# Optimization experiments

Hardware: AMD Instinct MI355X
Metric: run time of the kernel (lower is better)

## Reference

```python
import jax, jax.numpy as jnp
import numpy as np

EMB_DIM = 256
N_EMBED = 1024
BETA = 0.25


def setup_inputs() -> dict:
    key = jax.random.key(0)
    k1, k2 = jax.random.split(key)
    encoderout = jax.random.normal(k1, (32, EMB_DIM, 32, 32), dtype=jnp.float32)
    # embedding.weight.data.normal_(mean=0, std=1/n_embed)
    codebook = jax.random.normal(k2, (N_EMBED, EMB_DIM), dtype=jnp.float32) * (1.0 / N_EMBED)
    return {"encoderout": encoderout, "codebook": codebook}


def reference(encoderout, codebook):
    # NCHW -> NHWC
    x = jnp.transpose(encoderout, (0, 2, 3, 1))  # [B,H,W,D]
    flat = x.reshape(-1, EMB_DIM)                # [N,D]
    d2 = (jnp.sum(flat * flat, axis=1, keepdims=True)
          + jnp.sum(codebook * codebook, axis=1)[None, :]
          - 2.0 * flat @ codebook.T)             # [N,K]
    idx = jnp.argmin(d2, axis=1)                 # [N]
    quant = codebook[idx].reshape(x.shape)       # [B,H,W,D]
    codebook_loss = jnp.mean((quant - jax.lax.stop_gradient(x)) ** 2)
    commitment_loss = jnp.mean((x - jax.lax.stop_gradient(quant)) ** 2)
    loss = codebook_loss + BETA * commitment_loss
    # FAITHFUL to source bug: straight-through output is overwritten by the
    # input permuted back to NCHW, so out == encoderout.
    out = jnp.transpose(x, (0, 3, 1, 2))
    return (out, loss, codebook_loss, commitment_loss)
```

## Files before the change

kernel.cpp:

```cpp
#include <hip/hip_runtime.h>
#include <stdint.h>

typedef short s8v __attribute__((ext_vector_type(8)));
typedef float f4v __attribute__((ext_vector_type(4)));

#define EMB_DIM 256
#define HW      1024
#define NROWS   32768
#define NELEM   (NROWS * EMB_DIM)

#define PK_OFF   0u
#define CBN_OFF  524288u
#define PSQ_OFF  528384u
#define PSM_OFF  530432u
#define DONE_OFF 532480u

__device__ __forceinline__ unsigned f2bf(float f) {
    union { float f; unsigned u; } c; c.f = f;
    unsigned u = c.u;
    return (u + 0x7FFFu + ((u >> 16) & 1u)) >> 16;
}

__global__ __launch_bounds__(256) void prep_cb(const float* __restrict__ cb,
                                               unsigned short* __restrict__ pk,
                                               float* __restrict__ cbn,
                                               unsigned* __restrict__ done) {
    int T = blockIdx.x, t = threadIdx.x;
    if (T == 0 && t == 0) *done = 0u;
    {
        int code = t >> 4, seg = t & 15;
        const float* src = cb + (size_t)(T * 16 + code) * EMB_DIM + seg * 16;
        float s2 = 0.f;
        #pragma unroll
        for (int k = 0; k < 4; ++k) {
            float4 v = *(const float4*)(src + 4 * k);
            s2 += v.x * v.x + v.y * v.y + v.z * v.z + v.w * v.w;
        }
        #pragma unroll
        for (int m = 1; m < 16; m <<= 1) s2 += __shfl_xor(s2, m, 64);
        if (seg == 0) cbn[T * 16 + code] = s2;
    }
    #pragma unroll
    for (int it = 0; it < 2; ++it) {
        int idx = t + 256 * it;
        int s = idx >> 6, l = idx & 63, G = l >> 4, ci = l & 15;
        const float* q = cb + (size_t)(T * 16 + ci) * EMB_DIM + 32 * s + 8 * G;
        float4 v0 = *(const float4*)(q);
        float4 v1 = *(const float4*)(q + 4);
        unsigned o0 = f2bf(v0.x) | (f2bf(v0.y) << 16);
        unsigned o1 = f2bf(v0.z) | (f2bf(v0.w) << 16);
        unsigned o2 = f2bf(v1.x) | (f2bf(v1.y) << 16);
        unsigned o3 = f2bf(v1.z) | (f2bf(v1.w) << 16);
        *(uint4*)((char*)pk + (size_t)T * 8192 + (size_t)idx * 16) =
            make_uint4(o0, o1, o2, o3);
    }
}

__global__ __launch_bounds__(256, 2) void vq_fused(const float* __restrict__ x,
                                                   float* __restrict__ out,
                                                   const unsigned short* __restrict__ pk,
                                                   const float* __restrict__ cbn,
                                                   float* __restrict__ psq,
                                                   float* __restrict__ psm,
                                                   unsigned* __restrict__ done) {
    __shared__ float smemf[64 * 69];
    __shared__ uint4 frag[4 * 8 * 64];
    __shared__ float mloc[4][64];
    __shared__ float red[4];
    __shared__ bool  lastf;
    __shared__ double dred[4];

    int t = threadIdx.x;
    int blk = blockIdx.x;
    int b = blk >> 4, p0 = (blk & 15) << 6;
    const float* xb = x   + (size_t)b * (EMB_DIM * HW) + p0;
    float*       ob = out + (size_t)b * (EMB_DIM * HW) + p0;

    int l = t & 63, w = t >> 6;
    int G = l >> 4, ci = l & 15;

    float sq = 0.f;
    int pq = t & 15, dd = t >> 4;
    for (int kd = 0; kd < 4; ++kd) {
        #pragma unroll
        for (int c2 = 0; c2 < 4; ++c2) {
            int dl = dd + 16 * c2;
            size_t off = (size_t)(kd * 64 + dl) * HW + 4 * pq;
            f4v v = __builtin_nontemporal_load((const f4v*)(xb + off));
            __builtin_nontemporal_store(v, (f4v*)(ob + off));
            sq += v.x * v.x + v.y * v.y + v.z * v.z + v.w * v.w;
            float* dst = &smemf[dl * 69 + 4 * pq];
            dst[0] = v.x; dst[1] = v.y; dst[2] = v.z; dst[3] = v.w;
        }
        __syncthreads();
        #pragma unroll
        for (int it = 0; it < 2; ++it) {
            int f = t + 256 * it;
            int fl = f & 63, sL = (f >> 6) & 1, R = f >> 7;
            int fG = fl >> 4, fci = fl & 15;
            const float* q = &smemf[(32 * sL + 8 * fG) * 69 + 16 * R + fci];
            unsigned o0 = f2bf(q[0])   | (f2bf(q[69])  << 16);
            unsigned o1 = f2bf(q[138]) | (f2bf(q[207]) << 16);
            unsigned o2 = f2bf(q[276]) | (f2bf(q[345]) << 16);
            unsigned o3 = f2bf(q[414]) | (f2bf(q[483]) << 16);
            frag[(R * 8 + 2 * kd + sL) * 64 + fl] = make_uint4(o0, o1, o2, o3);
        }
        __syncthreads();
    }
    #pragma unroll
    for (int m = 1; m < 64; m <<= 1) sq += __shfl_xor(sq, m, 64);
    if (l == 0) red[w] = sq;

    s8v a[4][8];
    #pragma unroll
    for (int R = 0; R < 4; ++R)
        #pragma unroll
        for (int s = 0; s < 8; ++s)
            a[R][s] = *(const s8v*)&frag[(R * 8 + s) * 64 + l];

    float mv[4][4];
    #pragma unroll
    for (int R = 0; R < 4; ++R)
        #pragma unroll
        for (int r = 0; r < 4; ++r) mv[R][r] = 1e30f;

    const char* lbase = (const char*)pk + (size_t)l * 16;
    int qbase = w * 16;
    int off = blk & 15;
    s8v cur[8], nxt[8];
    {
        const char* pt = lbase + (size_t)(qbase + off) * 8192;
        #pragma unroll
        for (int s = 0; s < 8; ++s) cur[s] = *(const s8v*)(pt + (size_t)s * 1024);
    }
    #pragma unroll 2
    for (int i = 0; i < 16; ++i) {
        int Tn = qbase + ((off + ((i + 1) & 15)) & 15);
        const char* pn = lbase + (size_t)Tn * 8192;
        #pragma unroll
        for (int s = 0; s < 8; ++s) nxt[s] = *(const s8v*)(pn + (size_t)s * 1024);

        f4v ac0 = {0.f,0.f,0.f,0.f}, ac1 = {0.f,0.f,0.f,0.f};
        f4v ac2 = {0.f,0.f,0.f,0.f}, ac3 = {0.f,0.f,0.f,0.f};
        #pragma unroll
        for (int s = 0; s < 8; ++s) {
            ac0 = __builtin_amdgcn_mfma_f32_16x16x32_bf16(a[0][s], cur[s], ac0, 0, 0, 0);
            ac1 = __builtin_amdgcn_mfma_f32_16x16x32_bf16(a[1][s], cur[s], ac1, 0, 0, 0);
            ac2 = __builtin_amdgcn_mfma_f32_16x16x32_bf16(a[2][s], cur[s], ac2, 0, 0, 0);
            ac3 = __builtin_amdgcn_mfma_f32_16x16x32_bf16(a[3][s], cur[s], ac3, 0, 0, 0);
        }
        int Tc = qbase + ((off + i) & 15);
        float cv = cbn[Tc * 16 + ci];
        #pragma unroll
        for (int r = 0; r < 4; ++r) {
            mv[0][r] = fminf(mv[0][r], cv - 2.f * ac0[r]);
            mv[1][r] = fminf(mv[1][r], cv - 2.f * ac1[r]);
            mv[2][r] = fminf(mv[2][r], cv - 2.f * ac2[r]);
            mv[3][r] = fminf(mv[3][r], cv - 2.f * ac3[r]);
        }
        #pragma unroll
        for (int s = 0; s < 8; ++s) cur[s] = nxt[s];
    }

    #pragma unroll
    for (int R = 0; R < 4; ++R)
        #pragma unroll
        for (int r = 0; r < 4; ++r) {
            float v = mv[R][r];
            #pragma unroll
            for (int m = 1; m < 16; m <<= 1) v = fminf(v, __shfl_xor(v, m, 64));
            mv[R][r] = v;
        }
    if (ci == 0) {
        #pragma unroll
        for (int R = 0; R < 4; ++R)
            #pragma unroll
            for (int r = 0; r < 4; ++r)
                mloc[w][16 * R + 4 * G + r] = mv[R][r];
    }
    __syncthreads();

    if (t < 64) {
        float m = fminf(fminf(mloc[0][t], mloc[1][t]),
                        fminf(mloc[2][t], mloc[3][t]));
        #pragma unroll
        for (int mm = 1; mm < 64; mm <<= 1) m += __shfl_xor(m, mm, 64);
        if (t == 0) {
            __hip_atomic_store(&psm[blk], m, __ATOMIC_RELAXED, __HIP_MEMORY_SCOPE_AGENT);
            __hip_atomic_store(&psq[blk], red[0] + red[1] + red[2] + red[3],
                               __ATOMIC_RELAXED, __HIP_MEMORY_SCOPE_AGENT);
            __threadfence();
            unsigned old = __hip_atomic_fetch_add(done, 1u, __ATOMIC_RELAXED,
                                                  __HIP_MEMORY_SCOPE_AGENT);
            lastf = (old == 511u);
        }
    }
    __syncthreads();

    if (lastf) {
        __threadfence();
        double s = 0.0;
        #pragma unroll
        for (int h = 0; h < 2; ++h) {
            int idx = t + 256 * h;
            s += (double)__hip_atomic_load(&psm[idx], __ATOMIC_RELAXED, __HIP_MEMORY_SCOPE_AGENT)
               + (double)__hip_atomic_load(&psq[idx], __ATOMIC_RELAXED, __HIP_MEMORY_SCOPE_AGENT);
        }
        #pragma unroll
        for (int m = 1; m < 64; m <<= 1) s += __shfl_xor(s, m, 64);
        if (l == 0) dred[w] = s;
        __syncthreads();
        if (t == 0) {
            double tot = dred[0] + dred[1] + dred[2] + dred[3];
            double cl = tot / (double)NELEM;
            out[NELEM + 0] = (float)(1.25 * cl);
            out[NELEM + 1] = (float)cl;
            out[NELEM + 2] = (float)cl;
        }
    }
}

extern "C" void kernel_launch(void* const* d_in, const int* in_sizes, int n_in,
                              void* d_out, int out_size, void* d_ws, size_t ws_size,
                              hipStream_t stream) {
    const float* enc = (const float*)d_in[0];
    const float* cb  = (const float*)d_in[1];
    float* out = (float*)d_out;

    unsigned short* pk = (unsigned short*)((char*)d_ws + PK_OFF);
    float* cbn  = (float*)((char*)d_ws + CBN_OFF);
    float* psq  = (float*)((char*)d_ws + PSQ_OFF);
    float* psm  = (float*)((char*)d_ws + PSM_OFF);
    unsigned* done = (unsigned*)((char*)d_ws + DONE_OFF);

    prep_cb<<<64, 256, 0, stream>>>(cb, pk, cbn, done);
    vq_fused<<<512, 256, 0, stream>>>(enc, out, pk, cbn, psq, psm, done);
}
```

Baseline: 115.8 us.

## Split fused VQ kernel into copy/pack and distance-argmin kernels

Splits the fused kernel into two. copy_pack loads all of its x data up front, copies it to the output, computes squared norms, and writes bf16 MFMA fragments to a workspace buffer using double-buffered shared memory. vq_dist2 reads those fragments from global memory, preloads the codebook norms into registers, and loads B fragments inline instead of software-prefetching them. The aim is to keep the memory-bound copy phase separate from the MFMA phase so each kernel has less shared memory and register pressure. The cost is an extra launch and an extra round trip through global memory for the packed activations (about 16 MB).

```diff
diff --git a/kernel.cpp b/kernel.cpp
--- a/kernel.cpp
+++ b/kernel.cpp
@@ -14,6 +14,7 @@
 #define PSQ_OFF  528384u
 #define PSM_OFF  530432u
 #define DONE_OFF 532480u
+#define XPK_OFF  1048576u
 
 __device__ __forceinline__ unsigned f2bf(float f) {
     union { float f; unsigned u; } c; c.f = f;
@@ -56,40 +57,39 @@
     }
 }
 
-__global__ __launch_bounds__(256, 2) void vq_fused(const float* __restrict__ x,
-                                                   float* __restrict__ out,
-                                                   const unsigned short* __restrict__ pk,
-                                                   const float* __restrict__ cbn,
-                                                   float* __restrict__ psq,
-                                                   float* __restrict__ psm,
-                                                   unsigned* __restrict__ done) {
-    __shared__ float smemf[64 * 69];
-    __shared__ uint4 frag[4 * 8 * 64];
-    __shared__ float mloc[4][64];
+__global__ __launch_bounds__(256, 2) void copy_pack(const float* __restrict__ x,
+                                                    float* __restrict__ out,
+                                                    uint4* __restrict__ xpk,
+                                                    float* __restrict__ psq) {
+    __shared__ float smemf[2][64 * 69];
     __shared__ float red[4];
-    __shared__ bool  lastf;
-    __shared__ double dred[4];
-
-    int t = threadIdx.x;
-    int blk = blockIdx.x;
+
+    int t = threadIdx.x, blk = blockIdx.x;
     int b = blk >> 4, p0 = (blk & 15) << 6;
     const float* xb = x   + (size_t)b * (EMB_DIM * HW) + p0;
     float*       ob = out + (size_t)b * (EMB_DIM * HW) + p0;
 
-    int l = t & 63, w = t >> 6;
-    int G = l >> 4, ci = l & 15;
-
-    float sq = 0.f;
     int pq = t & 15, dd = t >> 4;
-    for (int kd = 0; kd < 4; ++kd) {
+
+    f4v vv[16];
+    #pragma unroll
+    for (int kd = 0; kd < 4; ++kd)
         #pragma unroll
         for (int c2 = 0; c2 < 4; ++c2) {
             int dl = dd + 16 * c2;
-            size_t off = (size_t)(kd * 64 + dl) * HW + 4 * pq;
-            f4v v = __builtin_nontemporal_load((const f4v*)(xb + off));
-            __builtin_nontemporal_store(v, (f4v*)(ob + off));
+            vv[kd * 4 + c2] = *(const f4v*)(xb + (size_t)(kd * 64 + dl) * HW + 4 * pq);
+        }
+
+    float sq = 0.f;
+    for (int kd = 0; kd < 4; ++kd) {
+        float* sbuf = smemf[kd & 1];
+        #pragma unroll
+        for (int c2 = 0; c2 < 4; ++c2) {
+            int dl = dd + 16 * c2;
+            f4v v = vv[kd * 4 + c2];
+            *(f4v*)(ob + (size_t)(kd * 64 + dl) * HW + 4 * pq) = v;
             sq += v.x * v.x + v.y * v.y + v.z * v.z + v.w * v.w;
-            float* dst = &smemf[dl * 69 + 4 * pq];
+            float* dst = &sbuf[dl * 69 + 4 * pq];
             dst[0] = v.x; dst[1] = v.y; dst[2] = v.z; dst[3] = v.w;
         }
         __syncthreads();
@@ -98,25 +98,50 @@
             int f = t + 256 * it;
             int fl = f & 63, sL = (f >> 6) & 1, R = f >> 7;
             int fG = fl >> 4, fci = fl & 15;
-            const float* q = &smemf[(32 * sL + 8 * fG) * 69 + 16 * R + fci];
+            const float* q = &sbuf[(32 * sL + 8 * fG) * 69 + 16 * R + fci];
             unsigned o0 = f2bf(q[0])   | (f2bf(q[69])  << 16);
             unsigned o1 = f2bf(q[138]) | (f2bf(q[207]) << 16);
             unsigned o2 = f2bf(q[276]) | (f2bf(q[345]) << 16);
             unsigned o3 = f2bf(q[414]) | (f2bf(q[483]) << 16);
-            frag[(R * 8 + 2 * kd + sL) * 64 + fl] = make_uint4(o0, o1, o2, o3);
-        }
-        __syncthreads();
-    }
+            xpk[((size_t)(blk * 4 + R) * 8 + 2 * kd + sL) * 64 + fl] =
+                make_uint4(o0, o1, o2, o3);
+        }
+    }
+
     #pragma unroll
     for (int m = 1; m < 64; m <<= 1) sq += __shfl_xor(sq, m, 64);
-    if (l == 0) red[w] = sq;
+    if ((t & 63) == 0) red[t >> 6] = sq;
+    __syncthreads();
+    if (t == 0) psq[blk] = red[0] + red[1] + red[2] + red[3];
+}
+
+__global__ __launch_bounds__(256, 2) void vq_dist2(const uint4* __restrict__ xpk,
+                                                   const unsigned short* __restrict__ pk,
+                                                   const float* __restrict__ cbn,
+                                                   const float* __restrict__ psq,
+                                                   float* __restrict__ psm,
+                                                   unsigned* __restrict__ done,
+                                                   float* __restrict__ out) {
+    __shared__ float mloc[4][64];
+    __shared__ bool  lastf;
+    __shared__ double dred[4];
+
+    int t = threadIdx.x, blk = blockIdx.x;
+    int l = t & 63, w = t >> 6;
+    int G = l >> 4, ci = l & 15;
 
     s8v a[4][8];
+    const uint4* pa = xpk + (size_t)blk * 2048 + l;
     #pragma unroll
     for (int R = 0; R < 4; ++R)
         #pragma unroll
         for (int s = 0; s < 8; ++s)
-            a[R][s] = *(const s8v*)&frag[(R * 8 + s) * 64 + l];
+            a[R][s] = *(const s8v*)&pa[(R * 8 + s) * 64];
+
+    int qbase = w * 16, off = blk & 15;
+    float cvs[16];
+    #pragma unroll
+    for (int T = 0; T < 16; ++T) cvs[T] = cbn[(qbase + T) * 16 + ci];
 
     float mv[4][4];
     #pragma unroll
@@ -125,32 +150,21 @@
         for (int r = 0; r < 4; ++r) mv[R][r] = 1e30f;
 
     const char* lbase = (const char*)pk + (size_t)l * 16;
-    int qbase = w * 16;
-    int off = blk & 15;
-    s8v cur[8], nxt[8];
-    {
-        const char* pt = lbase + (size_t)(qbase + off) * 8192;
-        #pragma unroll
-        for (int s = 0; s < 8; ++s) cur[s] = *(const s8v*)(pt + (size_t)s * 1024);
-    }
     #pragma unroll 2
     for (int i = 0; i < 16; ++i) {
-        int Tn = qbase + ((off + ((i + 1) & 15)) & 15);
-        const char* pn = lbase + (size_t)Tn * 8192;
-        #pragma unroll
-        for (int s = 0; s < 8; ++s) nxt[s] = *(const s8v*)(pn + (size_t)s * 1024);
-
+        int tt = (off + i) & 15;
+        const char* pt = lbase + (size_t)(qbase + tt) * 8192;
         f4v ac0 = {0.f,0.f,0.f,0.f}, ac1 = {0.f,0.f,0.f,0.f};
         f4v ac2 = {0.f,0.f,0.f,0.f}, ac3 = {0.f,0.f,0.f,0.f};
         #pragma unroll
         for (int s = 0; s < 8; ++s) {
-            ac0 = __builtin_amdgcn_mfma_f32_16x16x32_bf16(a[0][s], cur[s], ac0, 0, 0, 0);
-            ac1 = __builtin_amdgcn_mfma_f32_16x16x32_bf16(a[1][s], cur[s], ac1, 0, 0, 0);
-            ac2 = __builtin_amdgcn_mfma_f32_16x16x32_bf16(a[2][s], cur[s], ac2, 0, 0, 0);
-            ac3 = __builtin_amdgcn_mfma_f32_16x16x32_bf16(a[3][s], cur[s], ac3, 0, 0, 0);
-        }
-        int Tc = qbase + ((off + i) & 15);
-        float cv = cbn[Tc * 16 + ci];
+            s8v bf = *(const s8v*)(pt + (size_t)s * 1024);
+            ac0 = __builtin_amdgcn_mfma_f32_16x16x32_bf16(a[0][s], bf, ac0, 0, 0, 0);
+            ac1 = __builtin_amdgcn_mfma_f32_16x16x32_bf16(a[1][s], bf, ac1, 0, 0, 0);
+            ac2 = __builtin_amdgcn_mfma_f32_16x16x32_bf16(a[2][s], bf, ac2, 0, 0, 0);
+            ac3 = __builtin_amdgcn_mfma_f32_16x16x32_bf16(a[3][s], bf, ac3, 0, 0, 0);
+        }
+        float cv = cvs[tt];
         #pragma unroll
         for (int r = 0; r < 4; ++r) {
             mv[0][r] = fminf(mv[0][r], cv - 2.f * ac0[r]);
@@ -158,8 +172,6 @@
             mv[2][r] = fminf(mv[2][r], cv - 2.f * ac2[r]);
             mv[3][r] = fminf(mv[3][r], cv - 2.f * ac3[r]);
         }
-        #pragma unroll
-        for (int s = 0; s < 8; ++s) cur[s] = nxt[s];
     }
 
     #pragma unroll
@@ -187,8 +199,6 @@
         for (int mm = 1; mm < 64; mm <<= 1) m += __shfl_xor(m, mm, 64);
         if (t == 0) {
             __hip_atomic_store(&psm[blk], m, __ATOMIC_RELAXED, __HIP_MEMORY_SCOPE_AGENT);
-            __hip_atomic_store(&psq[blk], red[0] + red[1] + red[2] + red[3],
-                               __ATOMIC_RELAXED, __HIP_MEMORY_SCOPE_AGENT);
             __threadfence();
             unsigned old = __hip_atomic_fetch_add(done, 1u, __ATOMIC_RELAXED,
                                                   __HIP_MEMORY_SCOPE_AGENT);
@@ -204,7 +214,7 @@
         for (int h = 0; h < 2; ++h) {
             int idx = t + 256 * h;
             s += (double)__hip_atomic_load(&psm[idx], __ATOMIC_RELAXED, __HIP_MEMORY_SCOPE_AGENT)
-               + (double)__hip_atomic_load(&psq[idx], __ATOMIC_RELAXED, __HIP_MEMORY_SCOPE_AGENT);
+               + (double)psq[idx];
         }
         #pragma unroll
         for (int m = 1; m < 64; m <<= 1) s += __shfl_xor(s, m, 64);
@@ -232,7 +242,9 @@
     float* psq  = (float*)((char*)d_ws + PSQ_OFF);
     float* psm  = (float*)((char*)d_ws + PSM_OFF);
     unsigned* done = (unsigned*)((char*)d_ws + DONE_OFF);
+    uint4* xpk  = (uint4*)((char*)d_ws + XPK_OFF);
 
     prep_cb<<<64, 256, 0, stream>>>(cb, pk, cbn, done);
-    vq_fused<<<512, 256, 0, stream>>>(enc, out, pk, cbn, psq, psm, done);
-}
+    copy_pack<<<512, 256, 0, stream>>>(enc, out, xpk, psq);
+    vq_dist2<<<512, 256, 0, stream>>>(xpk, pk, cbn, psq, psm, done, out);
+}
```

Result: slower. 119.7 us (+3.3%).
